# Optimization experiments

Hardware: AMD Instinct MI355X
Metric: run time of the kernel (lower is better)

Reference implementation:

```python
import jax, jax.numpy as jnp
import numpy as np
from jax import lax

B, T, D_IN, D_CB, K_CB, H_MID = 32, 512, 1024, 256, 8192, 512

def setup_inputs() -> dict:
    key = jax.random.key(0)
    ks = jax.random.split(key, 12)
    s = 0.02
    return {
        "x": jax.random.normal(ks[0], (B, T, D_IN), jnp.float32),
        "w1": jax.random.normal(ks[1], (H_MID, D_IN), jnp.float32) * s,
        "b1": jnp.zeros((H_MID,), jnp.float32),
        "w2": jax.random.normal(ks[2], (D_CB, H_MID), jnp.float32) * s,
        "b2": jnp.zeros((D_CB,), jnp.float32),
        "conv_w": jax.random.normal(ks[3], (D_CB, D_CB, 3), jnp.float32) * s,
        "conv_b": jnp.zeros((D_CB,), jnp.float32),
        "codebook": jax.random.uniform(ks[4], (K_CB, D_CB), jnp.float32, -1.0 / K_CB, 1.0 / K_CB),
        "gru_wih": jax.random.normal(ks[5], (3 * D_CB, D_CB), jnp.float32) * s,
        "gru_whh": jax.random.normal(ks[6], (3 * D_CB, D_CB), jnp.float32) * s,
        "gru_bih": jnp.zeros((3 * D_CB,), jnp.float32),
        "gru_bhh": jnp.zeros((3 * D_CB,), jnp.float32),
    }

def _forward(x, w1, b1, w2, b2, conv_w, conv_b, codebook, gru_wih, gru_whh, gru_bih, gru_bhh):
    # feature_processor (dropout is identity at eval): [B,T,D_IN] -> [B,T,D_CB]
    h = jax.nn.relu(jnp.einsum('btd,hd->bth', x, w1) + b1)
    h = jax.nn.relu(jnp.einsum('bth,ch->btc', h, w2) + b2)
    # temporal conv1d, kernel 3, pad 1 (T > 1 here)
    f = jnp.transpose(h, (0, 2, 1))  # NCT
    f = lax.conv_general_dilated(f, conv_w, (1,), 'SAME', dimension_numbers=('NCH', 'OIH', 'NCH'))
    f = f + conv_b[None, :, None]
    features = jnp.transpose(f, (0, 2, 1))  # [B,T,D_CB]
    # quantize: squared-Euclidean nearest codebook entry (same argmin as cdist)
    flat = features.reshape(-1, features.shape[-1])  # [B*T, D_CB]
    d2 = (jnp.sum(flat * flat, axis=1, keepdims=True)
          - 2.0 * (flat @ codebook.T)
          + jnp.sum(codebook * codebook, axis=1))  # [B*T, K]
    idx = jnp.argmin(d2, axis=-1)
    quantized = codebook[idx].reshape(features.shape)  # [B,T,D_CB]
    token_indices = idx.reshape(features.shape[0], features.shape[1])
    commitment_loss = jnp.mean((features - lax.stop_gradient(quantized)) ** 2)
    codebook_loss = jnp.mean((quantized - lax.stop_gradient(features)) ** 2)
    # context predictor: 1-layer GRU over quantized[:, :-1]
    q_in = quantized[:, :-1]  # [B,T-1,D_CB]
    xproj = jnp.einsum('btd,hd->bth', q_in, gru_wih) + gru_bih  # [B,T-1,3H]
    Hd = quantized.shape[-1]
    def step(hprev, xt):
        gh = hprev @ gru_whh.T + gru_bhh  # [B,3H]
        xr, xz, xn = xt[:, :Hd], xt[:, Hd:2 * Hd], xt[:, 2 * Hd:]
        hr, hz, hn = gh[:, :Hd], gh[:, Hd:2 * Hd], gh[:, 2 * Hd:]
        r = jax.nn.sigmoid(xr + hr)
        z = jax.nn.sigmoid(xz + hz)
        n = jnp.tanh(xn + r * hn)
        hnew = (1.0 - z) * n + z * hprev
        return hnew, hnew
    h0 = jnp.zeros((q_in.shape[0], Hd), q_in.dtype)
    _, hs = lax.scan(step, h0, jnp.transpose(xproj, (1, 0, 2)))
    context = jnp.transpose(hs, (1, 0, 2))  # [B,T-1,D_CB]
    context_loss = jnp.mean((context - features[:, 1:]) ** 2)
    vq_loss = commitment_loss + 0.25 * codebook_loss + 0.1 * context_loss
    return token_indices, quantized, commitment_loss, codebook_loss, context_loss, vq_loss

def reference(x, w1, b1, w2, b2, conv_w, conv_b, codebook, gru_wih, gru_whh, gru_bih, gru_bhh):
    return _forward(x, w1, b1, w2, b2, conv_w, conv_b, codebook, gru_wih, gru_whh, gru_bih, gru_bhh)
```

## Files before the change

kernel.cpp:

```cpp
#include <hip/hip_runtime.h>
#include <math.h>

#define NB 32
#define NT 512
#define NDIN 1024
#define NDCB 256
#define NKCB 8192
#define NHMID 512
#define NROWS (NB*NT)

typedef _Float16 half2_t __attribute__((ext_vector_type(2)));
typedef __attribute__((ext_vector_type(8))) short bf16x8;
typedef __attribute__((ext_vector_type(8))) unsigned short u16x8;
typedef __attribute__((ext_vector_type(4))) float f32x4;

__device__ __forceinline__ unsigned short f2bf(float x) {
    unsigned int u = __float_as_uint(x);
    return (unsigned short)((u + 0x7fffu + ((u >> 16) & 1u)) >> 16);
}

#if __has_builtin(__builtin_amdgcn_fdot2)
__device__ __forceinline__ float dot2f(half2_t a, half2_t b, float c) {
    return __builtin_amdgcn_fdot2(a, b, c, false);
}
#else
__device__ __forceinline__ float dot2f(half2_t a, half2_t b, float c) {
    return fmaf((float)a[0], (float)b[0], fmaf((float)a[1], (float)b[1], c));
}
#endif

template<bool RELU>
__global__ __launch_bounds__(256) void gemm_nt_f64_kernel(
    const float* __restrict__ A, const float* __restrict__ Bm,
    const float* __restrict__ bias, float* __restrict__ C,
    int M, int N, int K)
{
    __shared__ double a_s[16*64];
    __shared__ double b_s[16*64];
    const int tid = threadIdx.x;
    const int bn0 = blockIdx.x * 64;
    const int bm0 = blockIdx.y * 64;
    const int lr = tid >> 2;
    const int kq = (tid & 3) << 2;
    const int tx = tid & 15, ty = tid >> 4;
    double acc[4][4] = {};
    const float* Ap = A + (size_t)(bm0 + lr) * K + kq;
    const float* Bp = Bm + (size_t)(bn0 + lr) * K + kq;
    for (int kt = 0; kt < K; kt += 16) {
        float4 a = *(const float4*)(Ap + kt);
        float4 b = *(const float4*)(Bp + kt);
        __syncthreads();
        a_s[(kq+0)*64+lr] = (double)a.x; a_s[(kq+1)*64+lr] = (double)a.y;
        a_s[(kq+2)*64+lr] = (double)a.z; a_s[(kq+3)*64+lr] = (double)a.w;
        b_s[(kq+0)*64+lr] = (double)b.x; b_s[(kq+1)*64+lr] = (double)b.y;
        b_s[(kq+2)*64+lr] = (double)b.z; b_s[(kq+3)*64+lr] = (double)b.w;
        __syncthreads();
        #pragma unroll
        for (int kk = 0; kk < 16; kk++) {
            double aa[4], bb[4];
            #pragma unroll
            for (int u = 0; u < 4; u++) { aa[u] = a_s[kk*64 + ty*4 + u]; bb[u] = b_s[kk*64 + tx*4 + u]; }
            #pragma unroll
            for (int i = 0; i < 4; i++)
                #pragma unroll
                for (int j = 0; j < 4; j++)
                    acc[i][j] = fma(aa[i], bb[j], acc[i][j]);
        }
    }
    const float4 b4 = *(const float4*)&bias[bn0 + tx*4];
    const double bc[4] = {(double)b4.x, (double)b4.y, (double)b4.z, (double)b4.w};
    #pragma unroll
    for (int i = 0; i < 4; i++) {
        float o[4];
        #pragma unroll
        for (int j = 0; j < 4; j++) {
            double v = acc[i][j] + bc[j];
            if (RELU) v = fmax(v, 0.0);
            o[j] = (float)v;
        }
        *(float4*)&C[(size_t)(bm0 + ty*4 + i)*N + bn0 + tx*4] =
            make_float4(o[0], o[1], o[2], o[3]);
    }
}

__global__ __launch_bounds__(256) void conv3_f64_kernel(
    const float* __restrict__ H2, const float* __restrict__ W3,
    const float* __restrict__ bias, float* __restrict__ F)
{
    __shared__ double a_s[16*68];
    __shared__ double b_s[3][16*64];
    const int tid = threadIdx.x;
    const int bn0 = blockIdx.x * 64;
    const int bm0 = blockIdx.y * 64;
    const int lr = tid >> 2;
    const int kq = (tid & 3) << 2;
    const int tx = tid & 15, ty = tid >> 4;
    const int tmod = bm0 & (NT-1);
    const bool has_top = (tmod != 0);
    const bool has_bot = (tmod + 64 < NT);
    double acc[4][4] = {};
    for (int kt = 0; kt < NDCB; kt += 16) {
        float4 a = make_float4(0.f,0.f,0.f,0.f);
        if (lr >= 1 || has_top)
            a = *(const float4*)&H2[(size_t)(bm0 - 1 + lr)*NDCB + kt + kq];
        float4 e = make_float4(0.f,0.f,0.f,0.f);
        int l2 = 0, kq2 = 0;
        if (tid < 8) {
            l2 = 64 + (tid >> 2); kq2 = (tid & 3) << 2;
            if (l2 == 64 || has_bot)
                e = *(const float4*)&H2[(size_t)(bm0 - 1 + l2)*NDCB + kt + kq2];
        }
        float4 w[3];
        #pragma unroll
        for (int s = 0; s < 3; s++)
            w[s] = *(const float4*)&W3[(size_t)s*65536 + (size_t)(bn0 + lr)*NDCB + kt + kq];
        __syncthreads();
        a_s[(kq+0)*68+lr]=(double)a.x; a_s[(kq+1)*68+lr]=(double)a.y;
        a_s[(kq+2)*68+lr]=(double)a.z; a_s[(kq+3)*68+lr]=(double)a.w;
        if (tid < 8) {
            a_s[(kq2+0)*68+l2]=(double)e.x; a_s[(kq2+1)*68+l2]=(double)e.y;
            a_s[(kq2+2)*68+l2]=(double)e.z; a_s[(kq2+3)*68+l2]=(double)e.w;
        }
        #pragma unroll
        for (int s = 0; s < 3; s++) {
            b_s[s][(kq+0)*64+lr]=(double)w[s].x; b_s[s][(kq+1)*64+lr]=(double)w[s].y;
            b_s[s][(kq+2)*64+lr]=(double)w[s].z; b_s[s][(kq+3)*64+lr]=(double)w[s].w;
        }
        __syncthreads();
        #pragma unroll
        for (int kk = 0; kk < 16; kk++) {
            double aa[6];
            #pragma unroll
            for (int u = 0; u < 6; u++) aa[u] = a_s[kk*68 + ty*4 + u];
            #pragma unroll
            for (int s = 0; s < 3; s++) {
                double bb[4];
                #pragma unroll
                for (int u = 0; u < 4; u++) bb[u] = b_s[s][kk*64 + tx*4 + u];
                #pragma unroll
                for (int i = 0; i < 4; i++)
                    #pragma unroll
                    for (int j = 0; j < 4; j++)
                        acc[i][j] = fma(aa[i+s], bb[j], acc[i][j]);
            }
        }
    }
    const float4 b4 = *(const float4*)&bias[bn0 + tx*4];
    const double bc[4] = {(double)b4.x, (double)b4.y, (double)b4.z, (double)b4.w};
    #pragma unroll
    for (int i = 0; i < 4; i++) {
        const size_t base = (size_t)(bm0 + ty*4 + i)*NDCB + bn0 + tx*4;
        *(float4*)&F[base] = make_float4((float)(acc[i][0]+bc[0]), (float)(acc[i][1]+bc[1]),
                                         (float)(acc[i][2]+bc[2]), (float)(acc[i][3]+bc[3]));
    }
}

__global__ __launch_bounds__(512) void vq_kernel(
    const float* __restrict__ F, const float* __restrict__ CB,
    const unsigned short* __restrict__ CBH,
    const float* __restrict__ cnorm, float* __restrict__ idx_out,
    float* __restrict__ qout, float* __restrict__ msd_acc)
{
    __shared__ unsigned short a_bf[64*256];
    __shared__ unsigned short b_bf[128*256];
    __shared__ float cn_s[128];
    __shared__ float red_v[64*64];
    __shared__ int   red_i[64*64];
    __shared__ int   bests[64];
    __shared__ int   cand[64][12];
    __shared__ int   ccnt[64];
    const int tid = threadIdx.x;
    const int m0 = blockIdx.x * 64;

    #pragma unroll
    for (int u = 0; u < 4; u++) {
        int e = tid + u*512;
        int row = e >> 5, c = e & 31;
        const float* src = &F[(size_t)(m0+row)*NDCB + c*8];
        float4 f0 = *(const float4*)src;
        float4 f1 = *(const float4*)(src+4);
        u16x8 p;
        p[0]=f2bf(f0.x); p[1]=f2bf(f0.y); p[2]=f2bf(f0.z); p[3]=f2bf(f0.w);
        p[4]=f2bf(f1.x); p[5]=f2bf(f1.y); p[6]=f2bf(f1.z); p[7]=f2bf(f1.w);
        *(u16x8*)((char*)a_bf + row*512 + ((c*16) ^ ((row&7)<<4))) = p;
    }

    const int w = tid >> 6, lane = tid & 63;
    const int l15 = lane & 15, kg = lane >> 4;
    const int rbase = (w & 3) << 4, cbase = (w >> 2) << 6;
    const char* aP = (const char*)a_bf + (size_t)(rbase + l15)*512;
    const char* bP = (const char*)b_bf + (size_t)(cbase + l15)*512;
    const int swz = (lane & 7) << 4;

    float mv1[4], mv2[4]; int mi1[4], mi2[4];
    #pragma unroll
    for (int i = 0; i < 4; i++) { mv1[i]=3.0e38f; mv2[i]=3.0e38f; mi1[i]=0x7fffffff; mi2[i]=0x7fffffff; }

    for (int n0 = 0; n0 < NKCB; n0 += 128) {
        __syncthreads();
        #pragma unroll
        for (int u = 0; u < 8; u++) {
            int e = tid + u*512;
            int row = e >> 5, c = e & 31;
            u16x8 v = *(const u16x8*)&CBH[(size_t)(n0+row)*NDCB + c*8];
            *(u16x8*)((char*)b_bf + row*512 + ((c*16) ^ ((row&7)<<4))) = v;
        }
        if (tid < 128) cn_s[tid] = cnorm[n0 + tid];
        __syncthreads();
        f32x4 acc[4] = {{0.f,0.f,0.f,0.f},{0.f,0.f,0.f,0.f},{0.f,0.f,0.f,0.f},{0.f,0.f,0.f,0.f}};
        #pragma unroll
        for (int kt = 0; kt < 8; kt++) {
            const int ko = (kt*64 + kg*16) ^ swz;
            bf16x8 av = *(const bf16x8*)(aP + ko);
            #pragma unroll
            for (int f = 0; f < 4; f++) {
                bf16x8 bv = *(const bf16x8*)(bP + f*8192 + ko);
                acc[f] = __builtin_amdgcn_mfma_f32_16x16x32_bf16(av, bv, acc[f], 0, 0, 0);
            }
        }
        #pragma unroll
        for (int f = 0; f < 4; f++) {
            const int col = n0 + cbase + f*16 + l15;
            const float cnv = cn_s[cbase + f*16 + l15];
            #pragma unroll
            for (int i = 0; i < 4; i++) {
                float s = fmaf(-2.0f, acc[f][i], cnv);
                if (s < mv1[i]) { mv2[i]=mv1[i]; mi2[i]=mi1[i]; mv1[i]=s; mi1[i]=col; }
                else if (s < mv2[i]) { mv2[i]=s; mi2[i]=col; }
            }
        }
    }
    #pragma unroll
    for (int i = 0; i < 4; i++) {
        const int row = rbase + kg*4 + i;
        const int eb  = (w>>2)*32 + l15*2;
        red_v[row*64 + eb]   = mv1[i]; red_i[row*64 + eb]   = mi1[i];
        red_v[row*64 + eb+1] = mv2[i]; red_i[row*64 + eb+1] = mi2[i];
    }
    __syncthreads();
    if (tid < 64) {
        float bv = 3.0e38f; int bi = 0x7fffffff;
        for (int e = 0; e < 64; e++) {
            float v = red_v[tid*64 + e]; int ii = red_i[tid*64 + e];
            if (v < bv || (v == bv && ii < bi)) { bv = v; bi = ii; }
        }
        int cnt = 0;
        for (int e = 0; e < 64; e++) {
            if (red_v[tid*64 + e] < bv + 1.0e-5f) {
                if (cnt < 12) cand[tid][cnt] = red_i[tid*64 + e];
                cnt++;
            }
        }
        bests[tid] = bi;
        ccnt[tid] = (cnt > 12) ? 12 : cnt;
    }
    __syncthreads();
    {
        const int wid = tid >> 6, lane2 = tid & 63;
        for (int r = wid; r < 64; r += 8) {
            const int nc = ccnt[r];
            if (nc < 2) continue;
            double sf = 0.0;
            #pragma unroll
            for (int u = 0; u < 4; u++) {
                double fv = (double)F[(size_t)(m0+r)*NDCB + lane2*4 + u];
                sf = fma(fv, fv, sf);
            }
            #pragma unroll
            for (int off = 32; off > 0; off >>= 1) sf += __shfl_down(sf, off);
            const float sf32 = (float)sf;
            float bd2 = 0.0f; int bidx = 0x7fffffff;
            for (int c = 0; c < nc; c++) {
                const int k = cand[r][c];
                double g = 0.0;
                #pragma unroll
                for (int u = 0; u < 4; u++) {
                    double cv = (double)CB[(size_t)k*NDCB + lane2*4 + u];
                    double fv = (double)F[(size_t)(m0+r)*NDCB + lane2*4 + u];
                    g = fma(cv, fv, g);
                }
                #pragma unroll
                for (int off = 32; off > 0; off >>= 1) g += __shfl_down(g, off);
                if (lane2 == 0) {
                    const float G32 = (float)g;
                    const float t  = sf32 - 2.0f*G32;
                    const float d2 = t + cnorm[k];
                    if (c == 0 || d2 < bd2 || (d2 == bd2 && k < bidx)) { bd2 = d2; bidx = k; }
                }
            }
            if (lane2 == 0) bests[r] = bidx;
        }
    }
    __syncthreads();
    if (tid < 64) idx_out[m0 + tid] = (float)bests[tid];
    float lsum = 0.0f;
    #pragma unroll
    for (int s = 0; s < 8; s++) {
        int e = tid + s*512;
        int row = e >> 6, kqe = (e & 63) << 2;
        float4 q = *(const float4*)&CB[(size_t)bests[row]*NDCB + kqe];
        float4 f = *(const float4*)&F[(size_t)(m0+row)*NDCB + kqe];
        float dx=f.x-q.x, dy=f.y-q.y, dz=f.z-q.z, dw=f.w-q.w;
        lsum += dx*dx + dy*dy + dz*dz + dw*dw;
        *(float4*)&qout[(size_t)(m0+row)*NDCB + kqe] = q;
    }
    red_v[tid] = lsum;
    __syncthreads();
    for (int off = 256; off > 0; off >>= 1) {
        if (tid < off) red_v[tid] += red_v[tid + off];
        __syncthreads();
    }
    if (tid == 0) atomicAdd(msd_acc, red_v[0]);
}

__global__ __launch_bounds__(256) void gemm_nt_kernel(
    const float* __restrict__ A, const float* __restrict__ Bm,
    const float* __restrict__ bias, float* __restrict__ C,
    int M, int N, int K)
{
    __shared__ float a_s[16*64];
    __shared__ float b_s[16*64];
    const int tid = threadIdx.x;
    const int bn0 = blockIdx.x * 64;
    const int bm0 = blockIdx.y * 64;
    const int lr = tid >> 2;
    const int kq = (tid & 3) << 2;
    const int tx = tid & 15, ty = tid >> 4;
    float acc[4][4] = {};
    const float* Ap = A + (size_t)(bm0 + lr) * K + kq;
    const float* Bp = Bm + (size_t)(bn0 + lr) * K + kq;
    for (int kt = 0; kt < K; kt += 16) {
        float4 a = *(const float4*)(Ap + kt);
        float4 b = *(const float4*)(Bp + kt);
        __syncthreads();
        a_s[(kq+0)*64+lr] = a.x; a_s[(kq+1)*64+lr] = a.y;
        a_s[(kq+2)*64+lr] = a.z; a_s[(kq+3)*64+lr] = a.w;
        b_s[(kq+0)*64+lr] = b.x; b_s[(kq+1)*64+lr] = b.y;
        b_s[(kq+2)*64+lr] = b.z; b_s[(kq+3)*64+lr] = b.w;
        __syncthreads();
        #pragma unroll
        for (int kk = 0; kk < 16; kk++) {
            const float4 av = *(const float4*)&a_s[kk*64 + ty*4];
            const float4 bv = *(const float4*)&b_s[kk*64 + tx*4];
            const float aa[4] = {av.x, av.y, av.z, av.w};
            const float bb[4] = {bv.x, bv.y, bv.z, bv.w};
            #pragma unroll
            for (int i = 0; i < 4; i++)
                #pragma unroll
                for (int j = 0; j < 4; j++)
                    acc[i][j] = fmaf(aa[i], bb[j], acc[i][j]);
        }
    }
    const float4 b4 = *(const float4*)&bias[bn0 + tx*4];
    const float bc[4] = {b4.x, b4.y, b4.z, b4.w};
    #pragma unroll
    for (int i = 0; i < 4; i++) {
        *(float4*)&C[(size_t)(bm0 + ty*4 + i)*N + bn0 + tx*4] =
            make_float4(acc[i][0]+bc[0], acc[i][1]+bc[1], acc[i][2]+bc[2], acc[i][3]+bc[3]);
    }
}

__global__ __launch_bounds__(512, 1) void gru_kernel(
    const float* __restrict__ XP, const float* __restrict__ WHH,
    const float* __restrict__ bhh, const float* __restrict__ F,
    float* __restrict__ ctx_acc)
{
    __shared__ float part[3][2][256];
    __shared__ uint4 hpk[2][32];
    __shared__ float red[256];
    const int tid = threadIdx.x;
    const int b = blockIdx.x;
    const int j = tid & 255;
    const int q = tid >> 8;
    half2_t wr[64], wz[64], wn[64];
    {
        const float* rp = WHH + (size_t)j*256 + q*128;
        #pragma unroll
        for (int k = 0; k < 32; k++) {
            float4 vr = *(const float4*)(rp + 4*k);
            float4 vz = *(const float4*)(rp + 65536 + 4*k);
            float4 vn = *(const float4*)(rp + 131072 + 4*k);
            wr[2*k+0] = (half2_t){(_Float16)vr.x, (_Float16)vr.y};
            wr[2*k+1] = (half2_t){(_Float16)vr.z, (_Float16)vr.w};
            wz[2*k+0] = (half2_t){(_Float16)vz.x, (_Float16)vz.y};
            wz[2*k+1] = (half2_t){(_Float16)vz.z, (_Float16)vz.w};
            wn[2*k+0] = (half2_t){(_Float16)vn.x, (_Float16)vn.y};
            wn[2*k+1] = (half2_t){(_Float16)vn.z, (_Float16)vn.w};
        }
    }
    if (tid < 64) hpk[tid >> 5][tid & 31] = make_uint4(0u, 0u, 0u, 0u);
    const float bb0 = bhh[j], bb1 = bhh[256+j], bb2 = bhh[512+j];
    const float* xpb = XP + (size_t)b*NT*768;
    const float* fb  = F  + (size_t)b*NT*NDCB;
    float hprev = 0.0f, lsum = 0.0f;
    __syncthreads();
    int cur = 0;
    for (int t = 0; t < NT-1; t++) {
        float xr = 0.f, xz = 0.f, xn = 0.f, fv = 0.f;
        if (tid < 256) {
            const float* xp = xpb + (size_t)t*768;
            xr = xp[j]; xz = xp[256+j]; xn = xp[512+j];
            fv = fb[(size_t)(t+1)*NDCB + j];
        }
        float a0=0.f, c0=0.f, a1=0.f, c1=0.f, a2=0.f, c2=0.f;
        #pragma unroll
        for (int kk = 0; kk < 16; kk++) {
            uint4 hp = hpk[cur][q*16 + kk];
            half2_t h0 = __builtin_bit_cast(half2_t, hp.x);
            half2_t h1 = __builtin_bit_cast(half2_t, hp.y);
            half2_t h2 = __builtin_bit_cast(half2_t, hp.z);
            half2_t h3 = __builtin_bit_cast(half2_t, hp.w);
            a0 = dot2f(wr[4*kk+0], h0, a0); c0 = dot2f(wr[4*kk+1], h1, c0);
            a1 = dot2f(wz[4*kk+0], h0, a1); c1 = dot2f(wz[4*kk+1], h1, c1);
            a2 = dot2f(wn[4*kk+0], h0, a2); c2 = dot2f(wn[4*kk+1], h1, c2);
            a0 = dot2f(wr[4*kk+2], h2, a0); c0 = dot2f(wr[4*kk+3], h3, c0);
            a1 = dot2f(wz[4*kk+2], h2, a1); c1 = dot2f(wz[4*kk+3], h3, c1);
            a2 = dot2f(wn[4*kk+2], h2, a2); c2 = dot2f(wn[4*kk+3], h3, c2);
        }
        part[0][q][j] = a0 + c0; part[1][q][j] = a1 + c1; part[2][q][j] = a2 + c2;
        __syncthreads();
        if (tid < 256) {
            float ghr = part[0][0][j] + part[0][1][j] + bb0;
            float ghz = part[1][0][j] + part[1][1][j] + bb1;
            float ghn = part[2][0][j] + part[2][1][j] + bb2;
            float r = 1.0f/(1.0f + __expf(-(xr + ghr)));
            float z = 1.0f/(1.0f + __expf(-(xz + ghz)));
            float v = fmaf(r, ghn, xn);
            v = fminf(fmaxf(v, -12.0f), 12.0f);
            float ev = __expf(-2.0f*v);
            float n = (1.0f - ev)/(1.0f + ev);
            float hnew = (1.0f - z)*n + z*hprev;
            float d = hnew - fv;
            lsum = fmaf(d, d, lsum);
            float nb = __shfl_down(hnew, 1);
            if (!(j & 1)) {
                half2_t p; p[0] = (_Float16)hnew; p[1] = (_Float16)nb;
                ((unsigned int*)&hpk[cur ^ 1][0])[j >> 1] = __builtin_bit_cast(unsigned int, p);
            }
            hprev = hnew;
        }
        __syncthreads();
        cur ^= 1;
    }
    if (tid < 256) red[j] = lsum;
    __syncthreads();
    for (int off = 128; off > 0; off >>= 1) {
        if (tid < off) red[tid] += red[tid + off];
        __syncthreads();
    }
    if (tid == 0) atomicAdd(ctx_acc, red[0]);
}

__global__ __launch_bounds__(256) void prep_kernel(
    const float* __restrict__ conv_w, float* __restrict__ w3,
    float* __restrict__ accv)
{
    int e = blockIdx.x*256 + threadIdx.x;
    if (e == 0) { accv[0] = 0.0f; accv[1] = 0.0f; }
    {
        int k = e >> 16;
        int r = e & 65535;
        int c = r >> 8, i = r & 255;
        w3[e] = conv_w[(size_t)c*768 + i*3 + k];
    }
}

__global__ __launch_bounds__(256) void cb2bf_kernel(
    const float* __restrict__ cb, unsigned short* __restrict__ cbh)
{
    int e = (blockIdx.x*256 + threadIdx.x) * 4;
    float4 v = *(const float4*)&cb[e];
    unsigned short p0 = f2bf(v.x), p1 = f2bf(v.y), p2 = f2bf(v.z), p3 = f2bf(v.w);
    unsigned long long pk = (unsigned long long)p0 | ((unsigned long long)p1 << 16)
                          | ((unsigned long long)p2 << 32) | ((unsigned long long)p3 << 48);
    *(unsigned long long*)&cbh[e] = pk;
}

__global__ __launch_bounds__(64) void cnorm_kernel(
    const float* __restrict__ CB, float* __restrict__ cn)
{
    const int k = blockIdx.x;
    const int lane = threadIdx.x;
    float4 v = *(const float4*)&CB[(size_t)k*NDCB + lane*4];
    double s = (double)v.x*(double)v.x + (double)v.y*(double)v.y
             + (double)v.z*(double)v.z + (double)v.w*(double)v.w;
    #pragma unroll
    for (int off = 32; off > 0; off >>= 1) s += __shfl_down(s, off);
    if (lane == 0) cn[k] = (float)s;
}

__global__ void finalize_kernel(const float* __restrict__ acc, float* __restrict__ out)
{
    if (threadIdx.x == 0) {
        float msd = acc[0] * (1.0f/4194304.0f);
        float ctx = acc[1] * (1.0f/4184064.0f);
        out[0] = msd;
        out[1] = msd;
        out[2] = ctx;
        out[3] = 1.25f*msd + 0.1f*ctx;
    }
}

extern "C" void kernel_launch(void* const* d_in, const int* in_sizes, int n_in,
                              void* d_out, int out_size, void* d_ws, size_t ws_size,
                              hipStream_t stream) {
    const float* x      = (const float*)d_in[0];
    const float* w1     = (const float*)d_in[1];
    const float* b1     = (const float*)d_in[2];
    const float* w2     = (const float*)d_in[3];
    const float* b2     = (const float*)d_in[4];
    const float* conv_w = (const float*)d_in[5];
    const float* conv_b = (const float*)d_in[6];
    const float* cb     = (const float*)d_in[7];
    const float* wih    = (const float*)d_in[8];
    const float* whh    = (const float*)d_in[9];
    const float* bih    = (const float*)d_in[10];
    const float* bhh    = (const float*)d_in[11];
    float* out = (float*)d_out;

    char* ws = (char*)d_ws;
    float*  feat   = (float*)(ws + 0);
    float*  h1     = (float*)(ws + 16777216);
    float*  xproj  = (float*)(ws + 16777216);
    float*  h2     = (float*)(ws + 50331648);
    unsigned short* cbh = (unsigned short*)(ws + 50331648);
    float*  cn     = (float*)(ws + 67108864);
    float*  w3     = (float*)(ws + 67141632);
    float*  accv   = (float*)(ws + 68714496);

    float* idx_out = out;
    float* qout    = out + 16384;
    float* louts   = out + 16384 + 4194304;

    prep_kernel<<<768, 256, 0, stream>>>(conv_w, w3, accv);
    cnorm_kernel<<<NKCB, 64, 0, stream>>>(cb, cn);
    gemm_nt_f64_kernel<true ><<<dim3(NHMID/64, NROWS/64), 256, 0, stream>>>(x,  w1, b1, h1, NROWS, NHMID, NDIN);
    gemm_nt_f64_kernel<true ><<<dim3(NDCB/64,  NROWS/64), 256, 0, stream>>>(h1, w2, b2, h2, NROWS, NDCB, NHMID);
    conv3_f64_kernel<<<dim3(NDCB/64, NROWS/64), 256, 0, stream>>>(h2, w3, conv_b, feat);
    cb2bf_kernel<<<2048, 256, 0, stream>>>(cb, cbh);
    vq_kernel<<<NROWS/64, 512, 0, stream>>>(feat, cb, cbh, cn, idx_out, qout, accv);
    gemm_nt_kernel<<<dim3(768/64, NROWS/64), 256, 0, stream>>>(qout, wih, bih, xproj, NROWS, 768, NDCB);
    gru_kernel<<<NB, 512, 0, stream>>>(xproj, whh, bhh, feat, accv + 1);
    finalize_kernel<<<1, 64, 0, stream>>>(accv, louts);
}
```

Baseline: 1.894 ms.

## Compute GRU input projection with fp16 MFMA instead of scalar fp32 GEMM

Replaces the fp32 shared-memory SIMT GEMM for the GRU input projection with an MFMA f16 kernel. The quantized rows are scaled by 8192 and cast to fp16 into swizzled LDS, and W_ih is pre-converted to fp16 in prep_kernel. Each block holds a 64-row A tile and loops over N in 128-column chunks. This cuts compute time for the 16384x768x256 GEMM at the cost of fp16 rounding in the GRU inputs. It also changes the GRU kernel's occupancy hint to waves_per_eu(2,2).

Result: faster. 1.785 ms (-5.7%).

```diff
diff --git a/kernel.cpp b/kernel.cpp
--- a/kernel.cpp
+++ b/kernel.cpp
@@ -10,6 +10,7 @@
 #define NROWS (NB*NT)
 
 typedef _Float16 half2_t __attribute__((ext_vector_type(2)));
+typedef _Float16 f16x8 __attribute__((ext_vector_type(8)));
 typedef __attribute__((ext_vector_type(8))) short bf16x8;
 typedef __attribute__((ext_vector_type(8))) unsigned short u16x8;
 typedef __attribute__((ext_vector_type(4))) float f32x4;
@@ -313,54 +314,72 @@
     if (tid == 0) atomicAdd(msd_acc, red_v[0]);
 }
 
-__global__ __launch_bounds__(256) void gemm_nt_kernel(
-    const float* __restrict__ A, const float* __restrict__ Bm,
-    const float* __restrict__ bias, float* __restrict__ C,
-    int M, int N, int K)
-{
-    __shared__ float a_s[16*64];
-    __shared__ float b_s[16*64];
+__global__ __launch_bounds__(512) void xproj_mfma_kernel(
+    const float* __restrict__ Q, const unsigned short* __restrict__ WIHH,
+    const float* __restrict__ bias, float* __restrict__ C)
+{
+    __shared__ unsigned short a_h[64*256];
+    __shared__ unsigned short b_h[128*256];
     const int tid = threadIdx.x;
-    const int bn0 = blockIdx.x * 64;
-    const int bm0 = blockIdx.y * 64;
-    const int lr = tid >> 2;
-    const int kq = (tid & 3) << 2;
-    const int tx = tid & 15, ty = tid >> 4;
-    float acc[4][4] = {};
-    const float* Ap = A + (size_t)(bm0 + lr) * K + kq;
-    const float* Bp = Bm + (size_t)(bn0 + lr) * K + kq;
-    for (int kt = 0; kt < K; kt += 16) {
-        float4 a = *(const float4*)(Ap + kt);
-        float4 b = *(const float4*)(Bp + kt);
-        __syncthreads();
-        a_s[(kq+0)*64+lr] = a.x; a_s[(kq+1)*64+lr] = a.y;
-        a_s[(kq+2)*64+lr] = a.z; a_s[(kq+3)*64+lr] = a.w;
-        b_s[(kq+0)*64+lr] = b.x; b_s[(kq+1)*64+lr] = b.y;
-        b_s[(kq+2)*64+lr] = b.z; b_s[(kq+3)*64+lr] = b.w;
-        __syncthreads();
-        #pragma unroll
-        for (int kk = 0; kk < 16; kk++) {
-            const float4 av = *(const float4*)&a_s[kk*64 + ty*4];
-            const float4 bv = *(const float4*)&b_s[kk*64 + tx*4];
-            const float aa[4] = {av.x, av.y, av.z, av.w};
-            const float bb[4] = {bv.x, bv.y, bv.z, bv.w};
-            #pragma unroll
-            for (int i = 0; i < 4; i++)
-                #pragma unroll
-                for (int j = 0; j < 4; j++)
-                    acc[i][j] = fmaf(aa[i], bb[j], acc[i][j]);
-        }
-    }
-    const float4 b4 = *(const float4*)&bias[bn0 + tx*4];
-    const float bc[4] = {b4.x, b4.y, b4.z, b4.w};
-    #pragma unroll
-    for (int i = 0; i < 4; i++) {
-        *(float4*)&C[(size_t)(bm0 + ty*4 + i)*N + bn0 + tx*4] =
-            make_float4(acc[i][0]+bc[0], acc[i][1]+bc[1], acc[i][2]+bc[2], acc[i][3]+bc[3]);
-    }
-}
-
-__global__ __launch_bounds__(512, 1) void gru_kernel(
+    const int m0 = blockIdx.x * 64;
+
+    #pragma unroll
+    for (int u = 0; u < 4; u++) {
+        int e = tid + u*512;
+        int row = e >> 5, c = e & 31;
+        const float* src = &Q[(size_t)(m0+row)*NDCB + c*8];
+        float4 f0 = *(const float4*)src;
+        float4 f1 = *(const float4*)(src+4);
+        f16x8 p;
+        p[0]=(_Float16)(f0.x*8192.0f); p[1]=(_Float16)(f0.y*8192.0f);
+        p[2]=(_Float16)(f0.z*8192.0f); p[3]=(_Float16)(f0.w*8192.0f);
+        p[4]=(_Float16)(f1.x*8192.0f); p[5]=(_Float16)(f1.y*8192.0f);
+        p[6]=(_Float16)(f1.z*8192.0f); p[7]=(_Float16)(f1.w*8192.0f);
+        *(f16x8*)((char*)a_h + row*512 + ((c*16) ^ ((row&7)<<4))) = p;
+    }
+
+    const int w = tid >> 6, lane = tid & 63;
+    const int l15 = lane & 15, kg = lane >> 4;
+    const int rbase = (w & 3) << 4, cbase = (w >> 2) << 6;
+    const char* aP = (const char*)a_h + (size_t)(rbase + l15)*512;
+    const char* bP = (const char*)b_h + (size_t)(cbase + l15)*512;
+    const int swz = (lane & 7) << 4;
+
+    for (int n0 = 0; n0 < 768; n0 += 128) {
+        __syncthreads();
+        #pragma unroll
+        for (int u = 0; u < 8; u++) {
+            int e = tid + u*512;
+            int row = e >> 5, c = e & 31;
+            u16x8 v = *(const u16x8*)&WIHH[(size_t)(n0+row)*NDCB + c*8];
+            *(u16x8*)((char*)b_h + row*512 + ((c*16) ^ ((row&7)<<4))) = v;
+        }
+        __syncthreads();
+        f32x4 acc[4] = {{0.f,0.f,0.f,0.f},{0.f,0.f,0.f,0.f},{0.f,0.f,0.f,0.f},{0.f,0.f,0.f,0.f}};
+        #pragma unroll
+        for (int kt = 0; kt < 8; kt++) {
+            const int ko = (kt*64 + kg*16) ^ swz;
+            f16x8 av = *(const f16x8*)(aP + ko);
+            #pragma unroll
+            for (int f = 0; f < 4; f++) {
+                f16x8 bv = *(const f16x8*)(bP + f*8192 + ko);
+                acc[f] = __builtin_amdgcn_mfma_f32_16x16x32_f16(av, bv, acc[f], 0, 0, 0);
+            }
+        }
+        #pragma unroll
+        for (int f = 0; f < 4; f++) {
+            const int col = n0 + cbase + f*16 + l15;
+            const float bv = bias[col];
+            #pragma unroll
+            for (int i = 0; i < 4; i++) {
+                const int row = m0 + rbase + kg*4 + i;
+                C[(size_t)row*768 + col] = fmaf(acc[f][i], 1.0f/8192.0f, bv);
+            }
+        }
+    }
+}
+
+__global__ __launch_bounds__(512) __attribute__((amdgpu_waves_per_eu(2, 2))) void gru_kernel(
     const float* __restrict__ XP, const float* __restrict__ WHH,
     const float* __restrict__ bhh, const float* __restrict__ F,
     float* __restrict__ ctx_acc)
@@ -453,6 +472,7 @@
 
 __global__ __launch_bounds__(256) void prep_kernel(
     const float* __restrict__ conv_w, float* __restrict__ w3,
+    const float* __restrict__ wih, unsigned short* __restrict__ wihh,
     float* __restrict__ accv)
 {
     int e = blockIdx.x*256 + threadIdx.x;
@@ -462,6 +482,10 @@
         int r = e & 65535;
         int c = r >> 8, i = r & 255;
         w3[e] = conv_w[(size_t)c*768 + i*3 + k];
+    }
+    {
+        _Float16 h = (_Float16)wih[e];
+        wihh[e] = __builtin_bit_cast(unsigned short, h);
     }
 }
 
@@ -526,20 +550,21 @@
     unsigned short* cbh = (unsigned short*)(ws + 50331648);
     float*  cn     = (float*)(ws + 67108864);
     float*  w3     = (float*)(ws + 67141632);
+    unsigned short* wihh = (unsigned short*)(ws + 67928064);
     float*  accv   = (float*)(ws + 68714496);
 
     float* idx_out = out;
     float* qout    = out + 16384;
     float* louts   = out + 16384 + 4194304;
 
-    prep_kernel<<<768, 256, 0, stream>>>(conv_w, w3, accv);
+    prep_kernel<<<768, 256, 0, stream>>>(conv_w, w3, wih, wihh, accv);
     cnorm_kernel<<<NKCB, 64, 0, stream>>>(cb, cn);
     gemm_nt_f64_kernel<true ><<<dim3(NHMID/64, NROWS/64), 256, 0, stream>>>(x,  w1, b1, h1, NROWS, NHMID, NDIN);
     gemm_nt_f64_kernel<true ><<<dim3(NDCB/64,  NROWS/64), 256, 0, stream>>>(h1, w2, b2, h2, NROWS, NDCB, NHMID);
     conv3_f64_kernel<<<dim3(NDCB/64, NROWS/64), 256, 0, stream>>>(h2, w3, conv_b, feat);
     cb2bf_kernel<<<2048, 256, 0, stream>>>(cb, cbh);
     vq_kernel<<<NROWS/64, 512, 0, stream>>>(feat, cb, cbh, cn, idx_out, qout, accv);
-    gemm_nt_kernel<<<dim3(768/64, NROWS/64), 256, 0, stream>>>(qout, wih, bih, xproj, NROWS, 768, NDCB);
+    xproj_mfma_kernel<<<NROWS/64, 512, 0, stream>>>(qout, wihh, bih, xproj);
     gru_kernel<<<NB, 512, 0, stream>>>(xproj, whh, bhh, feat, accv + 1);
     finalize_kernel<<<1, 64, 0, stream>>>(accv, louts);
 }
```
